# Kernel tuning notes

Hardware: AMD Instinct MI355X
Metric: run time of the kernel (lower is better)

The kernel has to match this reference:

```python
import jax, jax.numpy as jnp
import numpy as np

H = 16   # num_heads
K = 2    # top_k experts per token


def _layer_norm(x, g, b, eps=1e-5):
    mu = jnp.mean(x, axis=-1, keepdims=True)
    var = jnp.mean(jnp.square(x - mu), axis=-1, keepdims=True)
    return (x - mu) * jax.lax.rsqrt(var + eps) * g + b


def setup_inputs() -> dict:
    key = jax.random.key(0)
    ks = jax.random.split(key, 8)
    B, S, D, E = 2, 2048, 1024, 8
    sc = 0.02
    return {
        "x": jax.random.normal(ks[0], (B, S, D), jnp.float32),
        "wq": jax.random.normal(ks[1], (D, D), jnp.float32) * sc,
        "wk": jax.random.normal(ks[2], (D, D), jnp.float32) * sc,
        "wv": jax.random.normal(ks[3], (D, D), jnp.float32) * sc,
        "wo": jax.random.normal(ks[4], (D, D), jnp.float32) * sc,
        "ln1_g": jnp.ones((D,), jnp.float32),
        "ln1_b": jnp.zeros((D,), jnp.float32),
        "ln2_g": jnp.ones((D,), jnp.float32),
        "ln2_b": jnp.zeros((D,), jnp.float32),
        "router_w": jax.random.normal(ks[5], (E, D), jnp.float32) * sc,
        "expert_w": jax.random.normal(ks[6], (E, D, D), jnp.float32) * sc,
    }


def reference(x, wq, wk, wv, wo, ln1_g, ln1_b, ln2_g, ln2_b, router_w, expert_w):
    B, S, D = x.shape
    E = expert_w.shape[0]
    hd = D // H

    # ---- attention sublayer: x = x + attn(norm1(x)) ----
    h = _layer_norm(x, ln1_g, ln1_b)
    q = (h @ wq.T).reshape(B, S, H, hd).transpose(0, 2, 1, 3)  # bhsd
    k = (h @ wk.T).reshape(B, S, H, hd).transpose(0, 2, 1, 3)
    v = (h @ wv.T).reshape(B, S, H, hd).transpose(0, 2, 1, 3)
    scores = jnp.einsum("bhqd,bhkd->bhqk", q, k) / jnp.sqrt(jnp.float32(hd))
    causal = jnp.tril(jnp.ones((S, S), dtype=bool))
    scores = jnp.where(causal, scores, jnp.finfo(scores.dtype).min)
    probs = jax.nn.softmax(scores, axis=-1)
    attn = jnp.einsum("bhqk,bhkd->bhqd", probs, v)
    attn = attn.transpose(0, 2, 1, 3).reshape(B, S, D) @ wo.T
    x = x + attn

    # ---- MoE sublayer: x = x + moe(norm2(x)) ----
    h2 = _layer_norm(x, ln2_g, ln2_b)
    logits = jnp.einsum("bsd,ed->bse", h2, router_w)          # [B,S,E]
    top_logits, top_ids = jax.lax.top_k(logits, K)            # [B,S,K]
    gates = jax.nn.softmax(top_logits, axis=-1)               # [B,S,K]
    # dense combine weights over experts (E is small): sum_k gate_k * onehot(id_k)
    combine = jnp.sum(jax.nn.one_hot(top_ids, E, dtype=h2.dtype) * gates[..., None], axis=-2)  # [B,S,E]
    # per-token matvec with expert weights: token @ W_e.T for each expert, then weighted sum
    y = jnp.einsum("bsd,eod->bseo", h2, expert_w)             # [B,S,E,D]
    moe_out = jnp.einsum("bse,bseo->bso", combine, y)
    return x + moe_out
```

## Files before the change

kernel.cpp:

```cpp
#include <hip/hip_runtime.h>
#include <hip/hip_bf16.h>
#include <cstdint>


typedef __bf16 bf16;
typedef __bf16 bf16x8 __attribute__((ext_vector_type(8)));
typedef __bf16 bf16x4 __attribute__((ext_vector_type(4)));
typedef float f32x4 __attribute__((ext_vector_type(4)));
typedef float f32x16 __attribute__((ext_vector_type(16)));

#define MFMA(a, b, c) __builtin_amdgcn_mfma_f32_16x16x32_bf16(a, b, c, 0, 0, 0)
#define MFMA32(a, b, c) __builtin_amdgcn_mfma_f32_32x32x16_bf16(a, b, c, 0, 0, 0)

__device__ __forceinline__ void gld16(void* lds, const void* g) {
  __builtin_amdgcn_global_load_lds(
      (const __attribute__((address_space(1))) void*)g,
      (__attribute__((address_space(3))) void*)lds, 16, 0, 0);
}

__device__ __forceinline__ uint32_t pack_hilo(float pv) {
  bf16 h = (bf16)pv;
  bf16 l = (bf16)(pv - (float)h);
  union { bf16 b[2]; uint32_t u; } cv;
  cv.b[0] = h; cv.b[1] = l;
  return cv.u;
}

__global__ void prep_weights(const float* __restrict__ wq, const float* __restrict__ wk,
                             const float* __restrict__ wv, const float* __restrict__ wo,
                             const float* __restrict__ expw,
                             bf16* __restrict__ wqh, bf16* __restrict__ wql,
                             bf16* __restrict__ wkh, bf16* __restrict__ wkl,
                             bf16* __restrict__ wvh, bf16* __restrict__ wvl,
                             bf16* __restrict__ woh, bf16* __restrict__ wol,
                             bf16* __restrict__ ewh) {
  int bid = blockIdx.x;
  if (bid < 4096) {
    int wsel = bid >> 10;
    const float* src = wsel == 0 ? wq : wsel == 1 ? wk : wsel == 2 ? wv : wo;
    bf16* hi = wsel == 0 ? wqh : wsel == 1 ? wkh : wsel == 2 ? wvh : woh;
    bf16* lo = wsel == 0 ? wql : wsel == 1 ? wkl : wsel == 2 ? wvl : wol;
    int i = ((bid & 1023) * 256 + threadIdx.x) * 4;
    float4 v = *(const float4*)(src + i);
    float a[4] = {v.x, v.y, v.z, v.w};
#pragma unroll
    for (int j = 0; j < 4; j++) {
      bf16 h = (bf16)a[j];
      hi[i + j] = h;
      lo[i + j] = (bf16)(a[j] - (float)h);
    }
  } else {
    int i = ((bid - 4096) * 256 + threadIdx.x) * 4;
    float4 v = *(const float4*)(expw + i);
    ewh[i] = (bf16)v.x; ewh[i + 1] = (bf16)v.y;
    ewh[i + 2] = (bf16)v.z; ewh[i + 3] = (bf16)v.w;
  }
}

__global__ void ln_split(const float* __restrict__ x, const float* __restrict__ g,
                         const float* __restrict__ b, bf16* __restrict__ hi,
                         bf16* __restrict__ lo) {
  int tok = blockIdx.x, t = threadIdx.x;
  float4 v = ((const float4*)(x + (size_t)tok * 1024))[t];
  float s = v.x + v.y + v.z + v.w;
  float ss = v.x * v.x + v.y * v.y + v.z * v.z + v.w * v.w;
#pragma unroll
  for (int o = 1; o < 64; o <<= 1) { s += __shfl_xor(s, o); ss += __shfl_xor(ss, o); }
  __shared__ float red[8];
  int w = t >> 6, lane = t & 63;
  if (lane == 0) { red[w] = s; red[4 + w] = ss; }
  __syncthreads();
  s = red[0] + red[1] + red[2] + red[3];
  ss = red[4] + red[5] + red[6] + red[7];
  float mu = s * (1.f / 1024.f);
  float rstd = rsqrtf(ss * (1.f / 1024.f) - mu * mu + 1e-5f);
  float4 gv = ((const float4*)g)[t], bv = ((const float4*)b)[t];
  float y[4] = {(v.x - mu) * rstd * gv.x + bv.x, (v.y - mu) * rstd * gv.y + bv.y,
                (v.z - mu) * rstd * gv.z + bv.z, (v.w - mu) * rstd * gv.w + bv.w};
  size_t o = (size_t)tok * 1024 + t * 4;
#pragma unroll
  for (int j = 0; j < 4; j++) {
    bf16 h = (bf16)y[j];
    hi[o + j] = h;
    lo[o + j] = (bf16)(y[j] - (float)h);
  }
}

__global__ void ln2route(const float* __restrict__ x1, const float* __restrict__ g,
                         const float* __restrict__ b, const float* __restrict__ rw,
                         bf16* __restrict__ h2h, int* __restrict__ eid,
                         float2* __restrict__ gout) {
  int tok = blockIdx.x, t = threadIdx.x;
  float4 v = ((const float4*)(x1 + (size_t)tok * 1024))[t];
  float s = v.x + v.y + v.z + v.w;
  float ss = v.x * v.x + v.y * v.y + v.z * v.z + v.w * v.w;
#pragma unroll
  for (int o = 1; o < 64; o <<= 1) { s += __shfl_xor(s, o); ss += __shfl_xor(ss, o); }
  __shared__ float red[8];
  __shared__ float h2s[1024];
  __shared__ float lg[8];
  int w = t >> 6, lane = t & 63;
  if (lane == 0) { red[w] = s; red[4 + w] = ss; }
  __syncthreads();
  s = red[0] + red[1] + red[2] + red[3];
  ss = red[4] + red[5] + red[6] + red[7];
  float mu = s * (1.f / 1024.f);
  float rstd = rsqrtf(ss * (1.f / 1024.f) - mu * mu + 1e-5f);
  float4 gv = ((const float4*)g)[t], bv = ((const float4*)b)[t];
  float4 y;
  y.x = (v.x - mu) * rstd * gv.x + bv.x;
  y.y = (v.y - mu) * rstd * gv.y + bv.y;
  y.z = (v.z - mu) * rstd * gv.z + bv.z;
  y.w = (v.w - mu) * rstd * gv.w + bv.w;
  ((float4*)h2s)[t] = y;
  size_t o = (size_t)tok * 1024 + t * 4;
  h2h[o] = (bf16)y.x; h2h[o + 1] = (bf16)y.y;
  h2h[o + 2] = (bf16)y.z; h2h[o + 3] = (bf16)y.w;
  __syncthreads();
  float a0 = 0.f, a1 = 0.f;
  const float4* r0 = (const float4*)(rw + (2 * w) * 1024);
  const float4* r1 = (const float4*)(rw + (2 * w + 1) * 1024);
#pragma unroll
  for (int it = 0; it < 4; it++) {
    float4 xv = ((const float4*)h2s)[lane + 64 * it];
    float4 w0 = r0[lane + 64 * it];
    float4 w1 = r1[lane + 64 * it];
    a0 += xv.x * w0.x + xv.y * w0.y + xv.z * w0.z + xv.w * w0.w;
    a1 += xv.x * w1.x + xv.y * w1.y + xv.z * w1.z + xv.w * w1.w;
  }
#pragma unroll
  for (int o2 = 1; o2 < 64; o2 <<= 1) {
    a0 += __shfl_xor(a0, o2);
    a1 += __shfl_xor(a1, o2);
  }
  if (lane == 0) { lg[2 * w] = a0; lg[2 * w + 1] = a1; }
  __syncthreads();
  if (t == 0) {
    int i0 = 0; float l0 = lg[0];
#pragma unroll
    for (int e = 1; e < 8; e++) if (lg[e] > l0) { l0 = lg[e]; i0 = e; }
    int i1 = -1; float l1 = -3e38f;
#pragma unroll
    for (int e = 0; e < 8; e++) if (e != i0 && lg[e] > l1) { l1 = lg[e]; i1 = e; }
    float e1 = __expf(l1 - l0);
    float den = 1.f + e1;
    eid[tok] = i0 | (i1 << 4);
    gout[tok] = make_float2(1.f / den, e1 / den);
  }
}

__global__ void build_lists(const int* __restrict__ eid,
                            const float2* __restrict__ gv,
                            int* __restrict__ tlist, float* __restrict__ glist,
                            int* __restrict__ cnt) {
  int e = blockIdx.x, t = threadIdx.x;
  int lane = t & 63, w = t >> 6;
  __shared__ int wt[4];
  int base = 0;
  for (int c = 0; c < 16; c++) {
    int tok = c * 256 + t;
    int pair = eid[tok];
    int e0 = pair & 15, e1 = pair >> 4;
    bool p = (e0 == e) || (e1 == e);
    float2 g2 = gv[tok];
    float gate = (e0 == e) ? g2.x : g2.y;
    unsigned long long m = __ballot(p);
    int rank = __popcll(m & ((1ull << lane) - 1ull));
    if (lane == 0) wt[w] = __popcll(m);
    __syncthreads();
    int off = base;
    for (int i = 0; i < w; i++) off += wt[i];
    if (p) {
      tlist[e * 4096 + off + rank] = tok;
      glist[e * 4096 + off + rank] = gate;
    }
    base += wt[0] + wt[1] + wt[2] + wt[3];
    __syncthreads();
  }
  if (t == 0) cnt[e] = base;
  int pad = (base + 127) & ~127;
  if (pad > 4096) pad = 4096;
  for (int i = base + t; i < pad; i += 256) {
    tlist[e * 4096 + i] = 0;
    glist[e * 4096 + i] = 0.f;
  }
}

__device__ __forceinline__ void gemm_core_split(
    const bf16* __restrict__ Ah, const bf16* __restrict__ Al,
    const bf16* __restrict__ Bh, const bf16* __restrict__ Bl, int m0, int n0,
    f32x4 (&acc)[4][4]) {
  __shared__ __align__(16) bf16 As_h[4096], As_l[4096], Bs_h[4096], Bs_l[4096];
  int t = threadIdx.x, lane = t & 63, w = t >> 6;
  int i0 = t, i1 = t + 256;
  const bf16* a0h = Ah + (size_t)(m0 + (i0 >> 2)) * 1024 + (i0 & 3) * 8;
  const bf16* a1h = Ah + (size_t)(m0 + (i1 >> 2)) * 1024 + (i1 & 3) * 8;
  const bf16* a0l = Al + (size_t)(m0 + (i0 >> 2)) * 1024 + (i0 & 3) * 8;
  const bf16* a1l = Al + (size_t)(m0 + (i1 >> 2)) * 1024 + (i1 & 3) * 8;
  const bf16* b0h = Bh + (size_t)(n0 + (i0 >> 2)) * 1024 + (i0 & 3) * 8;
  const bf16* b1h = Bh + (size_t)(n0 + (i1 >> 2)) * 1024 + (i1 & 3) * 8;
  const bf16* b0l = Bl + (size_t)(n0 + (i0 >> 2)) * 1024 + (i0 & 3) * 8;
  const bf16* b1l = Bl + (size_t)(n0 + (i1 >> 2)) * 1024 + (i1 & 3) * 8;
  int wm = (w >> 1) * 64, wn = (w & 1) * 64;
  int lr = lane & 15, lq = lane >> 4;
  for (int k0 = 0; k0 < 1024; k0 += 32) {
    __syncthreads();
    gld16(&As_h[i0 * 8], a0h + k0); gld16(&As_h[i1 * 8], a1h + k0);
    gld16(&As_l[i0 * 8], a0l + k0); gld16(&As_l[i1 * 8], a1l + k0);
    gld16(&Bs_h[i0 * 8], b0h + k0); gld16(&Bs_h[i1 * 8], b1h + k0);
    gld16(&Bs_l[i0 * 8], b0l + k0); gld16(&Bs_l[i1 * 8], b1l + k0);
    __syncthreads();
    bf16x8 ah[4], al4[4], bh[4], bl4[4];
#pragma unroll
    for (int i = 0; i < 4; i++) {
      ah[i]  = *(const bf16x8*)&As_h[(wm + i * 16 + lr) * 32 + lq * 8];
      al4[i] = *(const bf16x8*)&As_l[(wm + i * 16 + lr) * 32 + lq * 8];
      bh[i]  = *(const bf16x8*)&Bs_h[(wn + i * 16 + lr) * 32 + lq * 8];
      bl4[i] = *(const bf16x8*)&Bs_l[(wn + i * 16 + lr) * 32 + lq * 8];
    }
#pragma unroll
    for (int i = 0; i < 4; i++)
#pragma unroll
      for (int j = 0; j < 4; j++) {
        f32x4 c = acc[i][j];
        c = MFMA(ah[i], bh[j], c);
        c = MFMA(ah[i], bl4[j], c);
        c = MFMA(al4[i], bh[j], c);
        acc[i][j] = c;
      }
  }
}

__global__ __launch_bounds__(256, 2) void gemm_qkv(
    const bf16* __restrict__ hh, const bf16* __restrict__ hl,
    const bf16* __restrict__ wqh, const bf16* __restrict__ wql,
    const bf16* __restrict__ wkh, const bf16* __restrict__ wkl,
    const bf16* __restrict__ wvh, const bf16* __restrict__ wvl,
    bf16* __restrict__ qh, bf16* __restrict__ ql, bf16* __restrict__ kh,
    bf16* __restrict__ kl, bf16* __restrict__ vth, bf16* __restrict__ vtl) {
  int n0 = blockIdx.x * 128, m0 = blockIdx.y * 128, z = blockIdx.z;
  const bf16 *Bh = wqh, *Bl = wql;
  if (z == 1) { Bh = wkh; Bl = wkl; }
  if (z == 2) { Bh = wvh; Bl = wvl; }
  f32x4 acc[4][4];
#pragma unroll
  for (int i = 0; i < 4; i++)
#pragma unroll
    for (int j = 0; j < 4; j++) acc[i][j] = (f32x4){0.f, 0.f, 0.f, 0.f};
  gemm_core_split(hh, hl, Bh, Bl, m0, n0, acc);
  int t = threadIdx.x, lane = t & 63, w = t >> 6;
  int wm = (w >> 1) * 64, wn = (w & 1) * 64, lr = lane & 15, lq = lane >> 4;
  if (z < 2) {
    bf16* Oh = z == 0 ? qh : kh;
    bf16* Ol = z == 0 ? ql : kl;
    float scale = (z == 0) ? (0.125f * 1.44269504f) : 1.0f;
#pragma unroll
    for (int i = 0; i < 4; i++)
#pragma unroll
      for (int j = 0; j < 4; j++)
#pragma unroll
        for (int r = 0; r < 4; r++) {
          size_t row = m0 + wm + i * 16 + lq * 4 + r;
          int col = n0 + wn + j * 16 + lr;
          float v = acc[i][j][r] * scale;
          bf16 h = (bf16)v;
          Oh[row * 1024 + col] = h;
          Ol[row * 1024 + col] = (bf16)(v - (float)h);
        }
  } else {
    int bb = m0 >> 11;
    int srow0 = m0 & 2047;
#pragma unroll
    for (int i = 0; i < 4; i++)
#pragma unroll
      for (int j = 0; j < 4; j++) {
        int col = n0 + wn + j * 16 + lr;
        int head = col >> 6, d = col & 63;
        int s = srow0 + wm + i * 16 + lq * 4;
        bf16x4 hv, lv;
#pragma unroll
        for (int r = 0; r < 4; r++) {
          float v = acc[i][j][r];
          bf16 h = (bf16)v;
          hv[r] = h;
          lv[r] = (bf16)(v - (float)h);
        }
        size_t off = ((size_t)((bb * 16 + head) * 64 + d)) * 2048 + s;
        *(bf16x4*)(vth + off) = hv;
        *(bf16x4*)(vtl + off) = lv;
      }
  }
}

__global__ __launch_bounds__(256, 2) void gemm_wo(
    const bf16* __restrict__ ah, const bf16* __restrict__ al,
    const bf16* __restrict__ bh, const bf16* __restrict__ bl,
    const float* __restrict__ resid, float* __restrict__ outp) {
  int n0 = blockIdx.x * 128, m0 = blockIdx.y * 128;
  f32x4 acc[4][4];
#pragma unroll
  for (int i = 0; i < 4; i++)
#pragma unroll
    for (int j = 0; j < 4; j++) acc[i][j] = (f32x4){0.f, 0.f, 0.f, 0.f};
  gemm_core_split(ah, al, bh, bl, m0, n0, acc);
  int t = threadIdx.x, lane = t & 63, w = t >> 6;
  int wm = (w >> 1) * 64, wn = (w & 1) * 64, lr = lane & 15, lq = lane >> 4;
#pragma unroll
  for (int i = 0; i < 4; i++)
#pragma unroll
    for (int j = 0; j < 4; j++)
#pragma unroll
      for (int r = 0; r < 4; r++) {
        size_t row = m0 + wm + i * 16 + lq * 4 + r;
        int col = n0 + wn + j * 16 + lr;
        outp[row * 1024 + col] = resid[row * 1024 + col] + acc[i][j][r];
      }
}

__global__ __launch_bounds__(256, 3) void attn_fused(
    const bf16* __restrict__ qh, const bf16* __restrict__ ql,
    const bf16* __restrict__ kh, const bf16* __restrict__ kl,
    const bf16* __restrict__ vth, const bf16* __restrict__ vtl,
    bf16* __restrict__ oh, bf16* __restrict__ ol) {
  const int S = 2048, D = 1024;
  int y = blockIdx.y;
  int qt = (y < 8) ? (15 - y) : (y - 8);
  int hb = blockIdx.x;
  int head = hb & 15, b = hb >> 4;
  int qb = qt * 128;
  int t = threadIdx.x, lane = t & 63, w = t >> 6;
  int l31 = lane & 31, l5 = lane >> 5;
  int base = b * S, hcol = head * 64;

  __shared__ __align__(16) bf16 Kh_s[4096], Kl_s[4096];
  __shared__ __align__(16) bf16 Vh_s[4096], Vl_s[4096];
  __shared__ __align__(16) uint32_t Pp[4][32 * 36];

  bf16x8 qfh[4], qfl[4];
  {
    const bf16* p1 = qh + (size_t)(base + qb + w * 32 + l31) * D + hcol + l5 * 8;
    const bf16* p2 = ql + (size_t)(base + qb + w * 32 + l31) * D + hcol + l5 * 8;
#pragma unroll
    for (int c = 0; c < 4; c++) {
      qfh[c] = *(const bf16x8*)(p1 + 16 * c);
      qfl[c] = *(const bf16x8*)(p2 + 16 * c);
    }
  }
  f32x16 O0, O1;
  float lrow[16];
#pragma unroll
  for (int r = 0; r < 16; r++) { O0[r] = 0.f; O1[r] = 0.f; lrow[r] = 0.f; }

  int r0 = t >> 3, p0 = t & 7;
  int r1 = 32 + r0;
  int g0 = p0 ^ (r0 & 7);
  const bf16* k0hp = kh + (size_t)(base + r0) * D + hcol + g0 * 8;
  const bf16* k1hp = kh + (size_t)(base + r1) * D + hcol + g0 * 8;
  const bf16* k0lp = kl + (size_t)(base + r0) * D + hcol + g0 * 8;
  const bf16* k1lp = kl + (size_t)(base + r1) * D + hcol + g0 * 8;
  const bf16* v0hp = vth + (size_t)(hb * 64 + r0) * 2048 + g0 * 8;
  const bf16* v1hp = vth + (size_t)(hb * 64 + r1) * 2048 + g0 * 8;
  const bf16* v0lp = vtl + (size_t)(hb * 64 + r0) * 2048 + g0 * 8;
  const bf16* v1lp = vtl + (size_t)(hb * 64 + r1) * 2048 + g0 * 8;

  int qwmin = qb + w * 32;

  for (int kt = 0; kt <= qb + 64; kt += 64) {
    __syncthreads();
    gld16(&Kh_s[t * 8], k0hp + (size_t)kt * D);
    gld16(&Kh_s[2048 + t * 8], k1hp + (size_t)kt * D);
    gld16(&Kl_s[t * 8], k0lp + (size_t)kt * D);
    gld16(&Kl_s[2048 + t * 8], k1lp + (size_t)kt * D);
    gld16(&Vh_s[t * 8], v0hp + kt);
    gld16(&Vh_s[2048 + t * 8], v1hp + kt);
    gld16(&Vl_s[t * 8], v0lp + kt);
    gld16(&Vl_s[2048 + t * 8], v1lp + kt);
    __syncthreads();
    if (kt > qwmin + 31) continue;
    bool mask0 = (kt + 31 > qwmin);
    bool skip1 = (kt + 32 > qwmin + 31);
    bool mask1 = (kt + 63 > qwmin);
#pragma unroll
    for (int ktile = 0; ktile < 2; ktile++) {
      if (ktile == 1 && skip1) break;
      int keyr = ktile * 32 + l31;
      f32x16 sc;
#pragma unroll
      for (int r = 0; r < 16; r++) sc[r] = 0.f;
      __builtin_amdgcn_s_setprio(1);
#pragma unroll
      for (int c = 0; c < 4; c++) {
        int dg = ((2 * c + l5) ^ (keyr & 7)) * 8;
        bf16x8 kv = *(const bf16x8*)&Kh_s[keyr * 64 + dg];
        bf16x8 km = *(const bf16x8*)&Kl_s[keyr * 64 + dg];
        sc = MFMA32(qfh[c], kv, sc);
        sc = MFMA32(qfl[c], kv, sc);
        sc = MFMA32(qfh[c], km, sc);
      }
      __builtin_amdgcn_s_setprio(0);
      bool m = ktile ? mask1 : mask0;
      int keyg = kt + keyr;
      uint32_t* prow = &Pp[w][l31];
#pragma unroll
      for (int r = 0; r < 16; r++) {
        int qlocal = (r & 3) + 8 * (r >> 2) + 4 * l5;
        float sv = sc[r];
        if (m && keyg > qwmin + qlocal) sv = -30000.f;
        float pv = __builtin_amdgcn_exp2f(sv);
        lrow[r] += pv;
        prow[qlocal * 36] = pack_hilo(pv);
      }
#pragma unroll
      for (int c2 = 0; c2 < 2; c2++) {
        const uint32_t* pr = &Pp[w][l31 * 36 + 16 * c2 + l5 * 8];
        uint32_t pd[8];
        *(uint4*)&pd[0] = *(const uint4*)&pr[0];
        *(uint4*)&pd[4] = *(const uint4*)&pr[4];
        union { uint32_t u[4]; bf16x8 v; } ph_, pl_;
#pragma unroll
        for (int i = 0; i < 4; i++) {
          ph_.u[i] = __builtin_amdgcn_perm(pd[2 * i + 1], pd[2 * i], 0x05040100u);
          pl_.u[i] = __builtin_amdgcn_perm(pd[2 * i + 1], pd[2 * i], 0x07060302u);
        }
        __builtin_amdgcn_s_setprio(1);
#pragma unroll
        for (int dtile = 0; dtile < 2; dtile++) {
          int d = dtile * 32 + l31;
          int kg = ((4 * ktile + 2 * c2 + l5) ^ (d & 7)) * 8;
          bf16x8 vb = *(const bf16x8*)&Vh_s[d * 64 + kg];
          bf16x8 vm = *(const bf16x8*)&Vl_s[d * 64 + kg];
          if (dtile == 0) {
            O0 = MFMA32(ph_.v, vb, O0);
            O0 = MFMA32(pl_.v, vb, O0);
            O0 = MFMA32(ph_.v, vm, O0);
          } else {
            O1 = MFMA32(ph_.v, vb, O1);
            O1 = MFMA32(pl_.v, vb, O1);
            O1 = MFMA32(ph_.v, vm, O1);
          }
        }
        __builtin_amdgcn_s_setprio(0);
      }
    }
  }
#pragma unroll
  for (int r = 0; r < 16; r++) {
    float l = lrow[r];
    l += __shfl_xor(l, 1); l += __shfl_xor(l, 2); l += __shfl_xor(l, 4);
    l += __shfl_xor(l, 8); l += __shfl_xor(l, 16);
    float linv = 1.f / l;
    int qlocal = (r & 3) + 8 * (r >> 2) + 4 * l5;
    size_t tok = (size_t)(base + qb + w * 32 + qlocal);
    float v0 = O0[r] * linv;
    float v1 = O1[r] * linv;
    bf16 h0 = (bf16)v0, h1 = (bf16)v1;
    oh[tok * D + hcol + l31] = h0;
    ol[tok * D + hcol + l31] = (bf16)(v0 - (float)h0);
    oh[tok * D + hcol + 32 + l31] = h1;
    ol[tok * D + hcol + 32 + l31] = (bf16)(v1 - (float)h1);
  }
}

__global__ __launch_bounds__(256, 2) void gemm_moe(
    const bf16* __restrict__ A, const bf16* __restrict__ W,
    const int* __restrict__ tlist, const float* __restrict__ glist,
    const int* __restrict__ cnt, float* __restrict__ outp) {
  int e = blockIdx.z;
  int count = cnt[e];
  int m0 = blockIdx.y * 128;
  if (m0 >= count) return;
  int n0 = blockIdx.x * 128;
  const int* tl = tlist + e * 4096;
  const bf16* B = W + (size_t)e * 1024 * 1024;
  __shared__ __align__(16) bf16 As[4096], Bs[4096];
  int t = threadIdx.x, lane = t & 63, w = t >> 6;
  int i0 = t, i1 = t + 256;
  int ra = tl[m0 + (i0 >> 2)], rb = tl[m0 + (i1 >> 2)];
  const bf16* a0 = A + (size_t)ra * 1024 + (i0 & 3) * 8;
  const bf16* a1 = A + (size_t)rb * 1024 + (i1 & 3) * 8;
  const bf16* b0 = B + (size_t)(n0 + (i0 >> 2)) * 1024 + (i0 & 3) * 8;
  const bf16* b1 = B + (size_t)(n0 + (i1 >> 2)) * 1024 + (i1 & 3) * 8;
  int wm = (w >> 1) * 64, wn = (w & 1) * 64, lr = lane & 15, lq = lane >> 4;
  f32x4 acc[4][4];
#pragma unroll
  for (int i = 0; i < 4; i++)
#pragma unroll
    for (int j = 0; j < 4; j++) acc[i][j] = (f32x4){0.f, 0.f, 0.f, 0.f};
  for (int k0 = 0; k0 < 1024; k0 += 32) {
    __syncthreads();
    gld16(&As[i0 * 8], a0 + k0); gld16(&As[i1 * 8], a1 + k0);
    gld16(&Bs[i0 * 8], b0 + k0); gld16(&Bs[i1 * 8], b1 + k0);
    __syncthreads();
    bf16x8 af[4], bfr[4];
#pragma unroll
    for (int i = 0; i < 4; i++) {
      af[i] = *(const bf16x8*)&As[(wm + i * 16 + lr) * 32 + lq * 8];
      bfr[i] = *(const bf16x8*)&Bs[(wn + i * 16 + lr) * 32 + lq * 8];
    }
#pragma unroll
    for (int i = 0; i < 4; i++)
#pragma unroll
      for (int j = 0; j < 4; j++) acc[i][j] = MFMA(af[i], bfr[j], acc[i][j]);
  }
#pragma unroll
  for (int i = 0; i < 4; i++)
#pragma unroll
    for (int r = 0; r < 4; r++) {
      int slot = m0 + wm + i * 16 + lq * 4 + r;
      if (slot < count) {
        int tok = tl[slot];
        float gte = glist[e * 4096 + slot];
#pragma unroll
        for (int j = 0; j < 4; j++) {
          int col = n0 + wn + j * 16 + lr;
          atomicAdd(&outp[(size_t)tok * 1024 + col], gte * acc[i][j][r]);
        }
      }
    }
}

extern "C" void kernel_launch(void* const* d_in, const int* in_sizes, int n_in,
                              void* d_out, int out_size, void* d_ws, size_t ws_size,
                              hipStream_t stream) {
  (void)in_sizes; (void)n_in; (void)out_size; (void)ws_size;
  const float* x    = (const float*)d_in[0];
  const float* wq   = (const float*)d_in[1];
  const float* wk   = (const float*)d_in[2];
  const float* wv   = (const float*)d_in[3];
  const float* wo   = (const float*)d_in[4];
  const float* ln1g = (const float*)d_in[5];
  const float* ln1b = (const float*)d_in[6];
  const float* ln2g = (const float*)d_in[7];
  const float* ln2b = (const float*)d_in[8];
  const float* rw   = (const float*)d_in[9];
  const float* expw = (const float*)d_in[10];
  float* out = (float*)d_out;

  char* p = (char*)d_ws;
  auto take = [&](size_t bytes) -> char* {
    char* r = p;
    p += (bytes + 255) & ~(size_t)255;
    return r;
  };
  const size_t ND2 = 4096ull * 1024 * 2;
  const size_t WD2 = 1024ull * 1024 * 2;
  bf16* h_hi = (bf16*)take(ND2); bf16* h_lo = (bf16*)take(ND2);
  bf16* wqh = (bf16*)take(WD2); bf16* wql = (bf16*)take(WD2);
  bf16* wkh = (bf16*)take(WD2); bf16* wkl = (bf16*)take(WD2);
  bf16* wvh = (bf16*)take(WD2); bf16* wvl = (bf16*)take(WD2);
  bf16* woh = (bf16*)take(WD2); bf16* wol = (bf16*)take(WD2);
  bf16* q_hi = (bf16*)take(ND2); bf16* q_lo = (bf16*)take(ND2);
  bf16* k_hi = (bf16*)take(ND2); bf16* k_lo = (bf16*)take(ND2);
  bf16* vt_hi = (bf16*)take(ND2); bf16* vt_lo = (bf16*)take(ND2);
  bf16* a_hi = (bf16*)take(ND2); bf16* a_lo = (bf16*)take(ND2);
  bf16* h2h  = (bf16*)take(ND2);
  bf16* ewh  = (bf16*)take(8ull * 1024 * 1024 * 2);
  int*   tlist  = (int*)take(8ull * 4096 * 4);
  float* glist  = (float*)take(8ull * 4096 * 4);
  int*   cnt    = (int*)take(64);
  int*   reid   = (int*)take(4096 * 4);
  float2* rg    = (float2*)take(4096 * 8);

  prep_weights<<<12288, 256, 0, stream>>>(wq, wk, wv, wo, expw, wqh, wql, wkh,
                                          wkl, wvh, wvl, woh, wol, ewh);
  ln_split<<<4096, 256, 0, stream>>>(x, ln1g, ln1b, h_hi, h_lo);
  gemm_qkv<<<dim3(8, 32, 3), 256, 0, stream>>>(h_hi, h_lo, wqh, wql, wkh, wkl,
                                               wvh, wvl, q_hi, q_lo, k_hi, k_lo,
                                               vt_hi, vt_lo);
  attn_fused<<<dim3(32, 16), 256, 0, stream>>>(q_hi, q_lo, k_hi, k_lo, vt_hi,
                                               vt_lo, a_hi, a_lo);
  gemm_wo<<<dim3(8, 32), 256, 0, stream>>>(a_hi, a_lo, woh, wol, x, out);
  ln2route<<<4096, 256, 0, stream>>>(out, ln2g, ln2b, rw, h2h, reid, rg);
  build_lists<<<8, 256, 0, stream>>>(reid, rg, tlist, glist, cnt);
  gemm_moe<<<dim3(8, 32, 8), 256, 0, stream>>>(h2h, ewh, tlist, glist, cnt,
                                               out);
}
```

Baseline: 452.3 us.

## Split attention key tile across two wave groups with LDS reduction

Doubles the attention block to 512 threads so that each 32-row query chunk is handled by two waves, each processing one 32-key half of every 64-key tile. Partial O and row sums from the second half are combined through shared memory at the end. The goal is more waves in flight per block and less serial work per wave, at the cost of a larger LDS footprint (about 66KB), an extra reduction pass, and removal of the setprio hints.

New measurement: 445.0 us. No clear change (-1.6%).

```diff
diff --git a/kernel.cpp b/kernel.cpp
--- a/kernel.cpp
+++ b/kernel.cpp
@@ -317,7 +317,7 @@
       }
 }
 
-__global__ __launch_bounds__(256, 3) void attn_fused(
+__global__ __launch_bounds__(512, 4) void attn_fused(
     const bf16* __restrict__ qh, const bf16* __restrict__ ql,
     const bf16* __restrict__ kh, const bf16* __restrict__ kl,
     const bf16* __restrict__ vth, const bf16* __restrict__ vtl,
@@ -329,17 +329,21 @@
   int head = hb & 15, b = hb >> 4;
   int qb = qt * 128;
   int t = threadIdx.x, lane = t & 63, w = t >> 6;
+  int rc = w & 3, khf = w >> 2;
   int l31 = lane & 31, l5 = lane >> 5;
   int base = b * S, hcol = head * 64;
 
-  __shared__ __align__(16) bf16 Kh_s[4096], Kl_s[4096];
-  __shared__ __align__(16) bf16 Vh_s[4096], Vl_s[4096];
-  __shared__ __align__(16) uint32_t Pp[4][32 * 36];
+  __shared__ __align__(16) char smem[67584];
+  bf16* Kh_s = (bf16*)smem;
+  bf16* Kl_s = (bf16*)(smem + 8192);
+  bf16* Vh_s = (bf16*)(smem + 16384);
+  bf16* Vl_s = (bf16*)(smem + 24576);
+  uint32_t* Pp = (uint32_t*)(smem + 32768);
 
   bf16x8 qfh[4], qfl[4];
   {
-    const bf16* p1 = qh + (size_t)(base + qb + w * 32 + l31) * D + hcol + l5 * 8;
-    const bf16* p2 = ql + (size_t)(base + qb + w * 32 + l31) * D + hcol + l5 * 8;
+    const bf16* p1 = qh + (size_t)(base + qb + rc * 32 + l31) * D + hcol + l5 * 8;
+    const bf16* p2 = ql + (size_t)(base + qb + rc * 32 + l31) * D + hcol + l5 * 8;
 #pragma unroll
     for (int c = 0; c < 4; c++) {
       qfh[c] = *(const bf16x8*)(p1 + 16 * c);
@@ -351,113 +355,114 @@
 #pragma unroll
   for (int r = 0; r < 16; r++) { O0[r] = 0.f; O1[r] = 0.f; lrow[r] = 0.f; }
 
-  int r0 = t >> 3, p0 = t & 7;
-  int r1 = 32 + r0;
-  int g0 = p0 ^ (r0 & 7);
-  const bf16* k0hp = kh + (size_t)(base + r0) * D + hcol + g0 * 8;
-  const bf16* k1hp = kh + (size_t)(base + r1) * D + hcol + g0 * 8;
-  const bf16* k0lp = kl + (size_t)(base + r0) * D + hcol + g0 * 8;
-  const bf16* k1lp = kl + (size_t)(base + r1) * D + hcol + g0 * 8;
-  const bf16* v0hp = vth + (size_t)(hb * 64 + r0) * 2048 + g0 * 8;
-  const bf16* v1hp = vth + (size_t)(hb * 64 + r1) * 2048 + g0 * 8;
-  const bf16* v0lp = vtl + (size_t)(hb * 64 + r0) * 2048 + g0 * 8;
-  const bf16* v1lp = vtl + (size_t)(hb * 64 + r1) * 2048 + g0 * 8;
-
-  int qwmin = qb + w * 32;
+  int row = t >> 3, p0 = t & 7;
+  int g0 = p0 ^ (row & 7);
+  const bf16* khp = kh + (size_t)(base + row) * D + hcol + g0 * 8;
+  const bf16* klp = kl + (size_t)(base + row) * D + hcol + g0 * 8;
+  const bf16* vhp = vth + (size_t)(hb * 64 + row) * 2048 + g0 * 8;
+  const bf16* vlp = vtl + (size_t)(hb * 64 + row) * 2048 + g0 * 8;
+
+  int qwmin = qb + rc * 32;
+  uint32_t* Ppw = Pp + rc * (32 * 68);
 
   for (int kt = 0; kt <= qb + 64; kt += 64) {
     __syncthreads();
-    gld16(&Kh_s[t * 8], k0hp + (size_t)kt * D);
-    gld16(&Kh_s[2048 + t * 8], k1hp + (size_t)kt * D);
-    gld16(&Kl_s[t * 8], k0lp + (size_t)kt * D);
-    gld16(&Kl_s[2048 + t * 8], k1lp + (size_t)kt * D);
-    gld16(&Vh_s[t * 8], v0hp + kt);
-    gld16(&Vh_s[2048 + t * 8], v1hp + kt);
-    gld16(&Vl_s[t * 8], v0lp + kt);
-    gld16(&Vl_s[2048 + t * 8], v1lp + kt);
-    __syncthreads();
-    if (kt > qwmin + 31) continue;
-    bool mask0 = (kt + 31 > qwmin);
-    bool skip1 = (kt + 32 > qwmin + 31);
-    bool mask1 = (kt + 63 > qwmin);
-#pragma unroll
-    for (int ktile = 0; ktile < 2; ktile++) {
-      if (ktile == 1 && skip1) break;
-      int keyr = ktile * 32 + l31;
-      f32x16 sc;
-#pragma unroll
-      for (int r = 0; r < 16; r++) sc[r] = 0.f;
-      __builtin_amdgcn_s_setprio(1);
-#pragma unroll
-      for (int c = 0; c < 4; c++) {
-        int dg = ((2 * c + l5) ^ (keyr & 7)) * 8;
-        bf16x8 kv = *(const bf16x8*)&Kh_s[keyr * 64 + dg];
-        bf16x8 km = *(const bf16x8*)&Kl_s[keyr * 64 + dg];
-        sc = MFMA32(qfh[c], kv, sc);
-        sc = MFMA32(qfl[c], kv, sc);
-        sc = MFMA32(qfh[c], km, sc);
+    gld16(&Kh_s[t * 8], khp + (size_t)kt * D);
+    gld16(&Kl_s[t * 8], klp + (size_t)kt * D);
+    gld16(&Vh_s[t * 8], vhp + kt);
+    gld16(&Vl_s[t * 8], vlp + kt);
+    __syncthreads();
+    if (kt + khf * 32 > qwmin + 31) continue;
+    bool maskw = (kt + khf * 32 + 31 > qwmin);
+    int keyr = khf * 32 + l31;
+    f32x16 sc;
+#pragma unroll
+    for (int r = 0; r < 16; r++) sc[r] = 0.f;
+#pragma unroll
+    for (int c = 0; c < 4; c++) {
+      int dg = ((2 * c + l5) ^ (keyr & 7)) * 8;
+      bf16x8 kv = *(const bf16x8*)&Kh_s[keyr * 64 + dg];
+      bf16x8 km = *(const bf16x8*)&Kl_s[keyr * 64 + dg];
+      sc = MFMA32(qfh[c], kv, sc);
+      sc = MFMA32(qfl[c], kv, sc);
+      sc = MFMA32(qfh[c], km, sc);
+    }
+    int keyg = kt + keyr;
+    uint32_t* prow = &Ppw[khf * 32 + l31];
+#pragma unroll
+    for (int r = 0; r < 16; r++) {
+      int qlocal = (r & 3) + 8 * (r >> 2) + 4 * l5;
+      float sv = sc[r];
+      if (maskw && keyg > qwmin + qlocal) sv = -30000.f;
+      float pv = __builtin_amdgcn_exp2f(sv);
+      lrow[r] += pv;
+      prow[qlocal * 68] = pack_hilo(pv);
+    }
+#pragma unroll
+    for (int c2 = 0; c2 < 2; c2++) {
+      const uint32_t* pr = &Ppw[l31 * 68 + khf * 32 + 16 * c2 + l5 * 8];
+      uint32_t pd[8];
+      *(uint4*)&pd[0] = *(const uint4*)&pr[0];
+      *(uint4*)&pd[4] = *(const uint4*)&pr[4];
+      union { uint32_t u[4]; bf16x8 v; } ph_, pl_;
+#pragma unroll
+      for (int i = 0; i < 4; i++) {
+        ph_.u[i] = __builtin_amdgcn_perm(pd[2 * i + 1], pd[2 * i], 0x05040100u);
+        pl_.u[i] = __builtin_amdgcn_perm(pd[2 * i + 1], pd[2 * i], 0x07060302u);
       }
-      __builtin_amdgcn_s_setprio(0);
-      bool m = ktile ? mask1 : mask0;
-      int keyg = kt + keyr;
-      uint32_t* prow = &Pp[w][l31];
-#pragma unroll
-      for (int r = 0; r < 16; r++) {
-        int qlocal = (r & 3) + 8 * (r >> 2) + 4 * l5;
-        float sv = sc[r];
-        if (m && keyg > qwmin + qlocal) sv = -30000.f;
-        float pv = __builtin_amdgcn_exp2f(sv);
-        lrow[r] += pv;
-        prow[qlocal * 36] = pack_hilo(pv);
+#pragma unroll
+      for (int dtile = 0; dtile < 2; dtile++) {
+        int d = dtile * 32 + l31;
+        int kg = ((4 * khf + 2 * c2 + l5) ^ (d & 7)) * 8;
+        bf16x8 vb = *(const bf16x8*)&Vh_s[d * 64 + kg];
+        bf16x8 vm = *(const bf16x8*)&Vl_s[d * 64 + kg];
+        if (dtile == 0) {
+          O0 = MFMA32(ph_.v, vb, O0);
+          O0 = MFMA32(pl_.v, vb, O0);
+          O0 = MFMA32(ph_.v, vm, O0);
+        } else {
+          O1 = MFMA32(ph_.v, vb, O1);
+          O1 = MFMA32(pl_.v, vb, O1);
+          O1 = MFMA32(ph_.v, vm, O1);
+        }
       }
-#pragma unroll
-      for (int c2 = 0; c2 < 2; c2++) {
-        const uint32_t* pr = &Pp[w][l31 * 36 + 16 * c2 + l5 * 8];
-        uint32_t pd[8];
-        *(uint4*)&pd[0] = *(const uint4*)&pr[0];
-        *(uint4*)&pd[4] = *(const uint4*)&pr[4];
-        union { uint32_t u[4]; bf16x8 v; } ph_, pl_;
-#pragma unroll
-        for (int i = 0; i < 4; i++) {
-          ph_.u[i] = __builtin_amdgcn_perm(pd[2 * i + 1], pd[2 * i], 0x05040100u);
-          pl_.u[i] = __builtin_amdgcn_perm(pd[2 * i + 1], pd[2 * i], 0x07060302u);
-        }
-        __builtin_amdgcn_s_setprio(1);
-#pragma unroll
-        for (int dtile = 0; dtile < 2; dtile++) {
-          int d = dtile * 32 + l31;
-          int kg = ((4 * ktile + 2 * c2 + l5) ^ (d & 7)) * 8;
-          bf16x8 vb = *(const bf16x8*)&Vh_s[d * 64 + kg];
-          bf16x8 vm = *(const bf16x8*)&Vl_s[d * 64 + kg];
-          if (dtile == 0) {
-            O0 = MFMA32(ph_.v, vb, O0);
-            O0 = MFMA32(pl_.v, vb, O0);
-            O0 = MFMA32(ph_.v, vm, O0);
-          } else {
-            O1 = MFMA32(ph_.v, vb, O1);
-            O1 = MFMA32(pl_.v, vb, O1);
-            O1 = MFMA32(ph_.v, vm, O1);
-          }
-        }
-        __builtin_amdgcn_s_setprio(0);
-      }
-    }
-  }
-#pragma unroll
-  for (int r = 0; r < 16; r++) {
-    float l = lrow[r];
-    l += __shfl_xor(l, 1); l += __shfl_xor(l, 2); l += __shfl_xor(l, 4);
-    l += __shfl_xor(l, 8); l += __shfl_xor(l, 16);
-    float linv = 1.f / l;
-    int qlocal = (r & 3) + 8 * (r >> 2) + 4 * l5;
-    size_t tok = (size_t)(base + qb + w * 32 + qlocal);
-    float v0 = O0[r] * linv;
-    float v1 = O1[r] * linv;
-    bf16 h0 = (bf16)v0, h1 = (bf16)v1;
-    oh[tok * D + hcol + l31] = h0;
-    ol[tok * D + hcol + l31] = (bf16)(v0 - (float)h0);
-    oh[tok * D + hcol + 32 + l31] = h1;
-    ol[tok * D + hcol + 32 + l31] = (bf16)(v1 - (float)h1);
+    }
+  }
+  __syncthreads();
+  float* scr = (float*)smem;
+  int sidx = (rc * 64 + lane) * 48;
+  if (khf == 1) {
+#pragma unroll
+    for (int r = 0; r < 16; r++) {
+      scr[sidx + r] = O0[r];
+      scr[sidx + 16 + r] = O1[r];
+      scr[sidx + 32 + r] = lrow[r];
+    }
+  }
+  __syncthreads();
+  if (khf == 0) {
+#pragma unroll
+    for (int r = 0; r < 16; r++) {
+      O0[r] += scr[sidx + r];
+      O1[r] += scr[sidx + 16 + r];
+      lrow[r] += scr[sidx + 32 + r];
+    }
+#pragma unroll
+    for (int r = 0; r < 16; r++) {
+      float l = lrow[r];
+      l += __shfl_xor(l, 1); l += __shfl_xor(l, 2); l += __shfl_xor(l, 4);
+      l += __shfl_xor(l, 8); l += __shfl_xor(l, 16);
+      float linv = 1.f / l;
+      int qlocal = (r & 3) + 8 * (r >> 2) + 4 * l5;
+      size_t tok = (size_t)(base + qb + rc * 32 + qlocal);
+      float v0 = O0[r] * linv;
+      float v1 = O1[r] * linv;
+      bf16 h0 = (bf16)v0, h1 = (bf16)v1;
+      oh[tok * D + hcol + l31] = h0;
+      ol[tok * D + hcol + l31] = (bf16)(v0 - (float)h0);
+      oh[tok * D + hcol + 32 + l31] = h1;
+      ol[tok * D + hcol + 32 + l31] = (bf16)(v1 - (float)h1);
+    }
   }
 }
 
@@ -567,7 +572,7 @@
   gemm_qkv<<<dim3(8, 32, 3), 256, 0, stream>>>(h_hi, h_lo, wqh, wql, wkh, wkl,
                                                wvh, wvl, q_hi, q_lo, k_hi, k_lo,
                                                vt_hi, vt_lo);
-  attn_fused<<<dim3(32, 16), 256, 0, stream>>>(q_hi, q_lo, k_hi, k_lo, vt_hi,
+  attn_fused<<<dim3(32, 16), 512, 0, stream>>>(q_hi, q_lo, k_hi, k_lo, vt_hi,
                                                vt_lo, a_hi, a_lo);
   gemm_wo<<<dim3(8, 32), 256, 0, stream>>>(a_hi, a_lo, woh, wol, x, out);
   ln2route<<<4096, 256, 0, stream>>>(out, ln2g, ln2b, rw, h2h, reid, rg);
```

## Double-buffer K/V tiles and keep P in registers via transposed QK MFMA

Applied to the files above, without the earlier changes.

Rewrites the causal attention kernel's inner loop. K/V tiles are now double-buffered in LDS so the next tile's global-to-LDS load overlaps compute on the current one. The QK^T MFMA operands are swapped so each lane holds a key-column of scores and the P hi/lo fragments are packed in registers, removing the per-wave LDS round trip for P. Row sums are reduced through a small LDS array. It also drops the load-balanced q-tile ordering and lowers launch bounds from 3 to 2 blocks per SM, because the doubled LDS footprint cuts occupancy.

Result: faster. 417.7 us (-7.6%).

```diff
diff --git a/kernel.cpp b/kernel.cpp
--- a/kernel.cpp
+++ b/kernel.cpp
@@ -16,14 +16,6 @@
   __builtin_amdgcn_global_load_lds(
       (const __attribute__((address_space(1))) void*)g,
       (__attribute__((address_space(3))) void*)lds, 16, 0, 0);
-}
-
-__device__ __forceinline__ uint32_t pack_hilo(float pv) {
-  bf16 h = (bf16)pv;
-  bf16 l = (bf16)(pv - (float)h);
-  union { bf16 b[2]; uint32_t u; } cv;
-  cv.b[0] = h; cv.b[1] = l;
-  return cv.u;
 }
 
 __global__ void prep_weights(const float* __restrict__ wq, const float* __restrict__ wk,
@@ -317,14 +309,13 @@
       }
 }
 
-__global__ __launch_bounds__(256, 3) void attn_fused(
+__global__ __launch_bounds__(256, 2) void attn_fused(
     const bf16* __restrict__ qh, const bf16* __restrict__ ql,
     const bf16* __restrict__ kh, const bf16* __restrict__ kl,
     const bf16* __restrict__ vth, const bf16* __restrict__ vtl,
     bf16* __restrict__ oh, bf16* __restrict__ ol) {
   const int S = 2048, D = 1024;
-  int y = blockIdx.y;
-  int qt = (y < 8) ? (15 - y) : (y - 8);
+  int qt = 15 - blockIdx.y;
   int hb = blockIdx.x;
   int head = hb & 15, b = hb >> 4;
   int qb = qt * 128;
@@ -332,9 +323,9 @@
   int l31 = lane & 31, l5 = lane >> 5;
   int base = b * S, hcol = head * 64;
 
-  __shared__ __align__(16) bf16 Kh_s[4096], Kl_s[4096];
-  __shared__ __align__(16) bf16 Vh_s[4096], Vl_s[4096];
-  __shared__ __align__(16) uint32_t Pp[4][32 * 36];
+  __shared__ __align__(16) bf16 Kh_s[2][4096], Kl_s[2][4096];
+  __shared__ __align__(16) bf16 Vh_s[2][4096], Vl_s[2][4096];
+  __shared__ float Ls[128];
 
   bf16x8 qfh[4], qfl[4];
   {
@@ -347,109 +338,130 @@
     }
   }
   f32x16 O0, O1;
-  float lrow[16];
-#pragma unroll
-  for (int r = 0; r < 16; r++) { O0[r] = 0.f; O1[r] = 0.f; lrow[r] = 0.f; }
+  float lsum = 0.f;
+#pragma unroll
+  for (int r = 0; r < 16; r++) { O0[r] = 0.f; O1[r] = 0.f; }
 
   int r0 = t >> 3, p0 = t & 7;
-  int r1 = 32 + r0;
   int g0 = p0 ^ (r0 & 7);
   const bf16* k0hp = kh + (size_t)(base + r0) * D + hcol + g0 * 8;
-  const bf16* k1hp = kh + (size_t)(base + r1) * D + hcol + g0 * 8;
+  const bf16* k1hp = kh + (size_t)(base + 32 + r0) * D + hcol + g0 * 8;
   const bf16* k0lp = kl + (size_t)(base + r0) * D + hcol + g0 * 8;
-  const bf16* k1lp = kl + (size_t)(base + r1) * D + hcol + g0 * 8;
+  const bf16* k1lp = kl + (size_t)(base + 32 + r0) * D + hcol + g0 * 8;
   const bf16* v0hp = vth + (size_t)(hb * 64 + r0) * 2048 + g0 * 8;
-  const bf16* v1hp = vth + (size_t)(hb * 64 + r1) * 2048 + g0 * 8;
+  const bf16* v1hp = vth + (size_t)(hb * 64 + 32 + r0) * 2048 + g0 * 8;
   const bf16* v0lp = vtl + (size_t)(hb * 64 + r0) * 2048 + g0 * 8;
-  const bf16* v1lp = vtl + (size_t)(hb * 64 + r1) * 2048 + g0 * 8;
+  const bf16* v1lp = vtl + (size_t)(hb * 64 + 32 + r0) * 2048 + g0 * 8;
 
   int qwmin = qb + w * 32;
-
-  for (int kt = 0; kt <= qb + 64; kt += 64) {
-    __syncthreads();
-    gld16(&Kh_s[t * 8], k0hp + (size_t)kt * D);
-    gld16(&Kh_s[2048 + t * 8], k1hp + (size_t)kt * D);
-    gld16(&Kl_s[t * 8], k0lp + (size_t)kt * D);
-    gld16(&Kl_s[2048 + t * 8], k1lp + (size_t)kt * D);
-    gld16(&Vh_s[t * 8], v0hp + kt);
-    gld16(&Vh_s[2048 + t * 8], v1hp + kt);
-    gld16(&Vl_s[t * 8], v0lp + kt);
-    gld16(&Vl_s[2048 + t * 8], v1lp + kt);
-    __syncthreads();
-    if (kt > qwmin + 31) continue;
-    bool mask0 = (kt + 31 > qwmin);
-    bool skip1 = (kt + 32 > qwmin + 31);
-    bool mask1 = (kt + 63 > qwmin);
-#pragma unroll
-    for (int ktile = 0; ktile < 2; ktile++) {
-      if (ktile == 1 && skip1) break;
-      int keyr = ktile * 32 + l31;
-      f32x16 sc;
-#pragma unroll
-      for (int r = 0; r < 16; r++) sc[r] = 0.f;
-      __builtin_amdgcn_s_setprio(1);
-#pragma unroll
-      for (int c = 0; c < 4; c++) {
-        int dg = ((2 * c + l5) ^ (keyr & 7)) * 8;
-        bf16x8 kv = *(const bf16x8*)&Kh_s[keyr * 64 + dg];
-        bf16x8 km = *(const bf16x8*)&Kl_s[keyr * 64 + dg];
-        sc = MFMA32(qfh[c], kv, sc);
-        sc = MFMA32(qfl[c], kv, sc);
-        sc = MFMA32(qfh[c], km, sc);
-      }
-      __builtin_amdgcn_s_setprio(0);
-      bool m = ktile ? mask1 : mask0;
-      int keyg = kt + keyr;
-      uint32_t* prow = &Pp[w][l31];
-#pragma unroll
-      for (int r = 0; r < 16; r++) {
-        int qlocal = (r & 3) + 8 * (r >> 2) + 4 * l5;
-        float sv = sc[r];
-        if (m && keyg > qwmin + qlocal) sv = -30000.f;
-        float pv = __builtin_amdgcn_exp2f(sv);
-        lrow[r] += pv;
-        prow[qlocal * 36] = pack_hilo(pv);
-      }
-#pragma unroll
-      for (int c2 = 0; c2 < 2; c2++) {
-        const uint32_t* pr = &Pp[w][l31 * 36 + 16 * c2 + l5 * 8];
-        uint32_t pd[8];
-        *(uint4*)&pd[0] = *(const uint4*)&pr[0];
-        *(uint4*)&pd[4] = *(const uint4*)&pr[4];
-        union { uint32_t u[4]; bf16x8 v; } ph_, pl_;
-#pragma unroll
-        for (int i = 0; i < 4; i++) {
-          ph_.u[i] = __builtin_amdgcn_perm(pd[2 * i + 1], pd[2 * i], 0x05040100u);
-          pl_.u[i] = __builtin_amdgcn_perm(pd[2 * i + 1], pd[2 * i], 0x07060302u);
-        }
+  int nt = 2 * qt + 2;
+
+#define STAGE(kts, bb) do { \
+    gld16(&Kh_s[bb][t * 8], k0hp + (size_t)(kts) * D); \
+    gld16(&Kh_s[bb][2048 + t * 8], k1hp + (size_t)(kts) * D); \
+    gld16(&Kl_s[bb][t * 8], k0lp + (size_t)(kts) * D); \
+    gld16(&Kl_s[bb][2048 + t * 8], k1lp + (size_t)(kts) * D); \
+    gld16(&Vh_s[bb][t * 8], v0hp + (kts)); \
+    gld16(&Vh_s[bb][2048 + t * 8], v1hp + (kts)); \
+    gld16(&Vl_s[bb][t * 8], v0lp + (kts)); \
+    gld16(&Vl_s[bb][2048 + t * 8], v1lp + (kts)); \
+  } while (0)
+
+  STAGE(0, 0);
+  __syncthreads();
+
+  for (int ti = 0; ti < nt; ti++) {
+    int kt = ti * 64;
+    int bb = ti & 1;
+    if (ti + 1 < nt) STAGE((ti + 1) * 64, bb ^ 1);
+    if (kt <= qwmin + 31) {
+      bool skip1 = (kt + 32 > qwmin + 31);
+#pragma unroll
+      for (int ktile = 0; ktile < 2; ktile++) {
+        if (ktile == 1 && skip1) break;
+        bool maskt = (kt + 32 * ktile + 31 > qwmin);
+        int keyr = ktile * 32 + l31;
+        f32x16 sc;
+#pragma unroll
+        for (int r = 0; r < 16; r++) sc[r] = 0.f;
         __builtin_amdgcn_s_setprio(1);
 #pragma unroll
-        for (int dtile = 0; dtile < 2; dtile++) {
-          int d = dtile * 32 + l31;
-          int kg = ((4 * ktile + 2 * c2 + l5) ^ (d & 7)) * 8;
-          bf16x8 vb = *(const bf16x8*)&Vh_s[d * 64 + kg];
-          bf16x8 vm = *(const bf16x8*)&Vl_s[d * 64 + kg];
-          if (dtile == 0) {
-            O0 = MFMA32(ph_.v, vb, O0);
-            O0 = MFMA32(pl_.v, vb, O0);
-            O0 = MFMA32(ph_.v, vm, O0);
-          } else {
-            O1 = MFMA32(ph_.v, vb, O1);
-            O1 = MFMA32(pl_.v, vb, O1);
-            O1 = MFMA32(ph_.v, vm, O1);
-          }
+        for (int c = 0; c < 4; c++) {
+          int dg = ((2 * c + l5) ^ (keyr & 7)) * 8;
+          bf16x8 kv = *(const bf16x8*)&Kh_s[bb][keyr * 64 + dg];
+          bf16x8 km = *(const bf16x8*)&Kl_s[bb][keyr * 64 + dg];
+          sc = MFMA32(kv, qfh[c], sc);
+          sc = MFMA32(kv, qfl[c], sc);
+          sc = MFMA32(km, qfh[c], sc);
         }
         __builtin_amdgcn_s_setprio(0);
+        int kb0 = kt + 32 * ktile + 4 * l5;
+        int qg = qwmin + l31;
+        float pvv[16];
+#pragma unroll
+        for (int r = 0; r < 16; r++) {
+          int cst = (r & 3) + 8 * (r >> 2);
+          float sv = sc[r];
+          if (maskt && (kb0 + cst > qg)) sv = -30000.f;
+          float p = __builtin_amdgcn_exp2f(sv);
+          pvv[r] = p;
+          lsum += p;
+        }
+        uint32_t hw[4][2], lw[4][2];
+#pragma unroll
+        for (int o = 0; o < 4; o++)
+#pragma unroll
+          for (int j = 0; j < 2; j++) {
+            int ra = 4 * o + 2 * j;
+            bf16 h0 = (bf16)pvv[ra], h1 = (bf16)pvv[ra + 1];
+            union { bf16 h[2]; uint32_t u; } ph, pl;
+            ph.h[0] = h0; ph.h[1] = h1;
+            pl.h[0] = (bf16)(pvv[ra] - (float)h0);
+            pl.h[1] = (bf16)(pvv[ra + 1] - (float)h1);
+            hw[o][j] = ph.u;
+            lw[o][j] = pl.u;
+          }
+#pragma unroll
+        for (int c2 = 0; c2 < 2; c2++) {
+          union { uint32_t u[4]; bf16x8 v; } pa, plo;
+          pa.u[0] = hw[2 * c2][0];     pa.u[1] = hw[2 * c2][1];
+          pa.u[2] = hw[2 * c2 + 1][0]; pa.u[3] = hw[2 * c2 + 1][1];
+          plo.u[0] = lw[2 * c2][0];     plo.u[1] = lw[2 * c2][1];
+          plo.u[2] = lw[2 * c2 + 1][0]; plo.u[3] = lw[2 * c2 + 1][1];
+          __builtin_amdgcn_s_setprio(1);
+#pragma unroll
+          for (int dtile = 0; dtile < 2; dtile++) {
+            int d = dtile * 32 + l31;
+            int gA = ((4 * ktile + 2 * c2) ^ (d & 7)) * 8 + 4 * l5;
+            int gB = ((4 * ktile + 2 * c2 + 1) ^ (d & 7)) * 8 + 4 * l5;
+            union { bf16x4 q[2]; bf16x8 v; } vbu, vmu;
+            vbu.q[0] = *(const bf16x4*)&Vh_s[bb][d * 64 + gA];
+            vbu.q[1] = *(const bf16x4*)&Vh_s[bb][d * 64 + gB];
+            vmu.q[0] = *(const bf16x4*)&Vl_s[bb][d * 64 + gA];
+            vmu.q[1] = *(const bf16x4*)&Vl_s[bb][d * 64 + gB];
+            if (dtile == 0) {
+              O0 = MFMA32(pa.v, vbu.v, O0);
+              O0 = MFMA32(plo.v, vbu.v, O0);
+              O0 = MFMA32(pa.v, vmu.v, O0);
+            } else {
+              O1 = MFMA32(pa.v, vbu.v, O1);
+              O1 = MFMA32(plo.v, vbu.v, O1);
+              O1 = MFMA32(pa.v, vmu.v, O1);
+            }
+          }
+          __builtin_amdgcn_s_setprio(0);
+        }
       }
     }
-  }
+    __syncthreads();
+  }
+#undef STAGE
+  float ltot = lsum + __shfl_xor(lsum, 32);
+  if (lane < 32) Ls[w * 32 + l31] = ltot;
 #pragma unroll
   for (int r = 0; r < 16; r++) {
-    float l = lrow[r];
-    l += __shfl_xor(l, 1); l += __shfl_xor(l, 2); l += __shfl_xor(l, 4);
-    l += __shfl_xor(l, 8); l += __shfl_xor(l, 16);
-    float linv = 1.f / l;
     int qlocal = (r & 3) + 8 * (r >> 2) + 4 * l5;
+    float linv = 1.f / Ls[w * 32 + qlocal];
     size_t tok = (size_t)(base + qb + w * 32 + qlocal);
     float v0 = O0[r] * linv;
     float v1 = O1[r] * linv;
```
